# Kernel optimization log

Hardware: AMD Instinct MI355X
Metric: run time of the kernel (lower is better)

## Reference

```python
import jax, jax.numpy as jnp
import numpy as np

CTX = 768   # ctx_len in the original module
C = 768     # n_embd
B = 16
T = 768
K_EPS = 1e-8


def setup_inputs() -> dict:
    key = jax.random.key(0)
    ks = jax.random.split(key, 10)
    scale = 1.0 / np.sqrt(C)
    x = jax.random.normal(ks[0], (B, T, C), jnp.float32)
    time_decay = jax.random.normal(ks[1], (C, 1), jnp.float32) * 0.1
    time_first = jnp.full((C, 1), np.log(0.3), jnp.float32)
    time_mix_k = jax.random.uniform(ks[2], (1, 1, C), jnp.float32)
    time_mix_v = jax.random.uniform(ks[3], (1, 1, C), jnp.float32)
    time_mix_r = jax.random.uniform(ks[4], (1, 1, C), jnp.float32)
    Wk = jax.random.normal(ks[5], (C, C), jnp.float32) * scale
    Wv = jax.random.normal(ks[6], (C, C), jnp.float32) * scale
    Wr = jax.random.normal(ks[7], (C, C), jnp.float32) * scale
    Wo = jax.random.normal(ks[8], (C, C), jnp.float32) * scale
    return {"x": x, "time_decay": time_decay, "time_first": time_first,
            "time_mix_k": time_mix_k, "time_mix_v": time_mix_v, "time_mix_r": time_mix_r,
            "Wk": Wk, "Wv": Wv, "Wr": Wr, "Wo": Wo}


def reference(x, time_decay, time_first, time_mix_k, time_mix_v, time_mix_r, Wk, Wv, Wr, Wo):
    Bb, Tt, Cc = x.shape
    # time_shift: xx[t] = x[t-1], xx[0] = 0
    xx = jnp.pad(x, ((0, 0), (1, 0), (0, 0)))[:, :Tt]
    xk = x * time_mix_k + xx * (1.0 - time_mix_k)
    xv = x * time_mix_v + xx * (1.0 - time_mix_v)
    xr = x * time_mix_r + xx * (1.0 - time_mix_r)
    # projections (nn.Linear, no bias: y = x @ W.T); k, v laid out [B, C, T]
    k = jnp.einsum('btc,oc->bot', xk, Wk)
    v = jnp.einsum('btc,oc->bot', xv, Wv)
    r = jnp.einsum('btc,oc->bto', xr, Wr)
    k = jnp.exp(jnp.minimum(k, 60.0))
    kv = k * v
    # decay kernel: time_w = cat([exp(time_decay)*time_curve, time_first]); w = exp(time_w)[:, -T:]
    curve = (jnp.arange(CTX - 1) - (CTX - 2)).astype(x.dtype)  # [-(CTX-2) .. 0]
    tw = jnp.concatenate([jnp.exp(time_decay) * curve[None, :], time_first], axis=-1)  # [C, CTX]
    w = jnp.exp(tw)[:, -Tt:]            # [C, T]
    kern = w[:, None, :]                # [C, 1, T] depthwise kernel

    def causal_conv(z):  # z: [B, C, T] -> [B, C, T], left-padded cross-correlation
        return jax.lax.conv_general_dilated(
            z, kern, window_strides=(1,), padding=[(Tt - 1, 0)],
            feature_group_count=Cc, dimension_numbers=('NCH', 'OIH', 'NCH'))

    wkv = causal_conv(kv)
    wk = causal_conv(k) + K_EPS
    rwkv = jax.nn.sigmoid(r) * jnp.transpose(wkv / wk, (0, 2, 1))  # [B, T, C]
    return jnp.einsum('btc,oc->bto', rwkv, Wo)
```

## Files before the change

### kernel.cpp

```cpp
#include <hip/hip_runtime.h>
#include <math.h>

#define Mq 12288
#define Nq 768
#define Kq 768
#define Tq 768
#define Bq 16
#define Cq 768
#define BK 64

typedef __bf16 bf16x8 __attribute__((ext_vector_type(8)));
typedef __bf16 bf16x4 __attribute__((ext_vector_type(4)));
typedef float  floatx4 __attribute__((ext_vector_type(4)));

#define GLD_LDS16(g, l) __builtin_amdgcn_global_load_lds(                      \
    (const __attribute__((address_space(1))) unsigned int*)(g),                \
    (__attribute__((address_space(3))) unsigned int*)(l), 16, 0, 0)

__global__ __launch_bounds__(256)
void prep_w(const float* __restrict__ Wk, const float* __restrict__ Wv,
            const float* __restrict__ Wr, const float* __restrict__ Wo,
            __bf16* __restrict__ o)
{
    const int i   = blockIdx.x * 256 + threadIdx.x;
    const int a   = i / 147456;
    const int off = (i - a * 147456) * 4;
    const float* s = (a == 0) ? Wk : (a == 1) ? Wv : (a == 2) ? Wr : Wo;
    const float4 v = *(const float4*)(s + off);
    bf16x4 r = { (__bf16)v.x, (__bf16)v.y, (__bf16)v.z, (__bf16)v.w };
    *(bf16x4*)(o + (size_t)a * 589824 + off) = r;
}

__global__ __launch_bounds__(256)
void prep_mix(const float* __restrict__ x,
              const float* __restrict__ mk, const float* __restrict__ mv,
              const float* __restrict__ mr,
              __bf16* __restrict__ xk, __bf16* __restrict__ xv,
              __bf16* __restrict__ xr)
{
    const int i  = blockIdx.x * 256 + threadIdx.x;
    const int c4 = i % (Cq / 4);
    const int m  = i / (Cq / 4);
    const int t  = m % Tq;
    const int c0 = c4 * 4;

    const float4 xc = *(const float4*)(x + (size_t)m * Cq + c0);
    float4 xp = make_float4(0.f, 0.f, 0.f, 0.f);
    if (t > 0) xp = *(const float4*)(x + (size_t)(m - 1) * Cq + c0);

    const float4 k4 = *(const float4*)(mk + c0);
    const float4 v4 = *(const float4*)(mv + c0);
    const float4 r4 = *(const float4*)(mr + c0);

    bf16x4 ok = { (__bf16)fmaf(k4.x, xc.x - xp.x, xp.x),
                  (__bf16)fmaf(k4.y, xc.y - xp.y, xp.y),
                  (__bf16)fmaf(k4.z, xc.z - xp.z, xp.z),
                  (__bf16)fmaf(k4.w, xc.w - xp.w, xp.w) };
    bf16x4 ov = { (__bf16)fmaf(v4.x, xc.x - xp.x, xp.x),
                  (__bf16)fmaf(v4.y, xc.y - xp.y, xp.y),
                  (__bf16)fmaf(v4.z, xc.z - xp.z, xp.z),
                  (__bf16)fmaf(v4.w, xc.w - xp.w, xp.w) };
    bf16x4 orr = { (__bf16)fmaf(r4.x, xc.x - xp.x, xp.x),
                   (__bf16)fmaf(r4.y, xc.y - xp.y, xp.y),
                   (__bf16)fmaf(r4.z, xc.z - xp.z, xp.z),
                   (__bf16)fmaf(r4.w, xc.w - xp.w, xp.w) };
    const size_t o = (size_t)m * Cq + c0;
    *(bf16x4*)(xk + o) = ok;
    *(bf16x4*)(xv + o) = ov;
    *(bf16x4*)(xr + o) = orr;
}

template<bool KVR>
__global__ __launch_bounds__(256)
void mfma_gemm(const __bf16* __restrict__ A0, const __bf16* __restrict__ A1,
               const __bf16* __restrict__ A2,
               const __bf16* __restrict__ W,
               __bf16* __restrict__ OUTb,
               float*  __restrict__ OUTf)
{
    __shared__ __bf16 As[128 * BK];
    __shared__ __bf16 Bs[128 * BK];

    const int tid   = threadIdx.x;
    const int wave  = tid >> 6;
    const int lane  = tid & 63;
    const int m0    = blockIdx.y * 128;
    const int nb    = blockIdx.x;
    const int matid = KVR ? nb / 6 : 0;
    const int n0    = KVR ? (nb % 6) * 128 : nb * 128;
    const int wn0   = nb * 128;

    const __bf16* A = KVR ? (matid == 0 ? A0 : matid == 1 ? A1 : A2) : A0;

    const int r8 = lane >> 3;
    const int cc = lane & 7;
    const int sc = cc ^ r8;
    const __bf16* gA[4];
    const __bf16* gB[4];
    __bf16* lA[4];
    __bf16* lB[4];
#pragma unroll
    for (int i = 0; i < 4; ++i) {
        const int row = (wave * 4 + i) * 8 + r8;
        gA[i] = A + (size_t)(m0  + row) * Kq + sc * 8;
        gB[i] = W + (size_t)(wn0 + row) * Kq + sc * 8;
        lA[i] = As + (wave * 4 + i) * 512;
        lB[i] = Bs + (wave * 4 + i) * 512;
    }

    const int qr = wave >> 1, qc = wave & 1;
    const int rowA = qr * 64 + (lane & 15);
    const int rowB = qc * 64 + (lane & 15);
    const int lk   = lane >> 4;

    floatx4 acc[4][4];
#pragma unroll
    for (int i = 0; i < 4; ++i)
#pragma unroll
        for (int j = 0; j < 4; ++j) acc[i][j] = (floatx4){0.f, 0.f, 0.f, 0.f};

    for (int kt = 0; kt < Kq / BK; ++kt) {
#pragma unroll
        for (int i = 0; i < 4; ++i) {
            GLD_LDS16(gA[i], lA[i]);
            GLD_LDS16(gB[i], lB[i]);
            gA[i] += BK; gB[i] += BK;
        }
        __syncthreads();

#pragma unroll
        for (int kk = 0; kk < 2; ++kk) {
            bf16x8 aF[4], bF[4];
#pragma unroll
            for (int i = 0; i < 4; ++i) {
                const int ra = rowA + i * 16;
                aF[i] = *(const bf16x8*)(As + ra * BK +
                                         (((kk << 2) | lk) ^ (ra & 7)) * 8);
            }
#pragma unroll
            for (int j = 0; j < 4; ++j) {
                const int rb = rowB + j * 16;
                bF[j] = *(const bf16x8*)(Bs + rb * BK +
                                         (((kk << 2) | lk) ^ (rb & 7)) * 8);
            }
#pragma unroll
            for (int i = 0; i < 4; ++i)
#pragma unroll
                for (int j = 0; j < 4; ++j)
                    acc[i][j] = __builtin_amdgcn_mfma_f32_16x16x32_bf16(
                        aF[i], bF[j], acc[i][j], 0, 0, 0);
        }
        __syncthreads();
    }

    const int er = qr * 64 + (lane >> 4) * 4;
    const int ec = qc * 64 + (lane & 15);
#pragma unroll
    for (int i = 0; i < 4; ++i) {
#pragma unroll
        for (int j = 0; j < 4; ++j) {
            const int n = n0 + ec + j * 16;
#pragma unroll
            for (int reg = 0; reg < 4; ++reg) {
                const int m = m0 + er + i * 16 + reg;
                float v = acc[i][j][reg];
                if (KVR) {
                    if (matid == 0)      v = expf(fminf(v, 60.f));
                    else if (matid == 2) v = 1.f / (1.f + expf(-v));
                    OUTb[(size_t)matid * Mq * Nq + (size_t)m * Nq + n] = (__bf16)v;
                } else {
                    OUTf[(size_t)m * Nq + n] = v;
                }
            }
        }
    }
}

#define SEG 8
#define SLEN (Tq / SEG)

__global__ __launch_bounds__(512)
void scan_kernel(const __bf16* __restrict__ kb, const __bf16* __restrict__ vb,
                 __bf16* rb,
                 const float* __restrict__ td, const float* __restrict__ tf)
{
    __shared__ float aS[SEG][64];
    __shared__ float bS[SEG][64];

    const int cx  = threadIdx.x;
    const int seg = threadIdx.y;
    const int c   = blockIdx.x * 64 + cx;
    const int b   = blockIdx.y;

    const float d  = expf(td[c]);
    const float wd = expf(-d);
    const float u  = expf(tf[c]);

    const size_t base = ((size_t)b * Tq + seg * SLEN) * Cq + c;

    float a = 0.f, bs = 0.f;
    for (int t = 0; t < SLEN; ++t) {
        const size_t idx = base + (size_t)t * Cq;
        const float kt = (float)kb[idx];
        const float vt = (float)vb[idx];
        a  = fmaf(wd, a, kt * vt);
        bs = fmaf(wd, bs, kt);
    }
    aS[seg][cx] = a;
    bS[seg][cx] = bs;
    __syncthreads();

    if (seg == 0) {
        const float w96 = expf(-d * (float)SLEN);
        float ina = 0.f, inb = 0.f;
#pragma unroll
        for (int s = 0; s < SEG; ++s) {
            const float ta = aS[s][cx];
            const float tb = bS[s][cx];
            aS[s][cx] = ina;
            bS[s][cx] = inb;
            ina = fmaf(w96, ina, ta);
            inb = fmaf(w96, inb, tb);
        }
    }
    __syncthreads();

    a  = aS[seg][cx];
    bs = bS[seg][cx];
    for (int t = 0; t < SLEN; ++t) {
        const size_t idx = base + (size_t)t * Cq;
        const float kt = (float)kb[idx];
        const float vt = (float)vb[idx];
        const float sr = (float)rb[idx];
        const float kv = kt * vt;
        const float num = fmaf(u, kv, a);
        const float den = fmaf(u, kt, bs) + 1e-8f;
        rb[idx] = (__bf16)(sr * num / den);
        a  = fmaf(wd, a, kv);
        bs = fmaf(wd, bs, kt);
    }
}

extern "C" void kernel_launch(void* const* d_in, const int* in_sizes, int n_in,
                              void* d_out, int out_size, void* d_ws, size_t ws_size,
                              hipStream_t stream)
{
    const float* x  = (const float*)d_in[0];
    const float* td = (const float*)d_in[1];
    const float* tf = (const float*)d_in[2];
    const float* mk = (const float*)d_in[3];
    const float* mv = (const float*)d_in[4];
    const float* mr = (const float*)d_in[5];
    const float* Wk = (const float*)d_in[6];
    const float* Wv = (const float*)d_in[7];
    const float* Wr = (const float*)d_in[8];
    const float* Wo = (const float*)d_in[9];

    const size_t MC = (size_t)Mq * Cq;

    __bf16* xk = (__bf16*)d_out;
    __bf16* xv = xk + MC;

    __bf16* xr   = (__bf16*)d_ws;
    __bf16* kbuf = xr + MC;
    __bf16* vbuf = kbuf + MC;
    __bf16* rbuf = vbuf + MC;
    __bf16* Wp   = rbuf + MC;
    __bf16* Wob  = Wp + 3 * 589824;

    prep_w<<<2304, 256, 0, stream>>>(Wk, Wv, Wr, Wo, Wp);
    prep_mix<<<(Mq * (Cq / 4)) / 256, 256, 0, stream>>>(x, mk, mv, mr, xk, xv, xr);

    mfma_gemm<true><<<dim3(18, 96), 256, 0, stream>>>(
        xk, xv, xr, Wp, kbuf, nullptr);

    scan_kernel<<<dim3(Cq / 64, Bq), dim3(64, SEG), 0, stream>>>(
        kbuf, vbuf, rbuf, td, tf);

    mfma_gemm<false><<<dim3(6, 96), 256, 0, stream>>>(
        rbuf, nullptr, nullptr, Wob, nullptr, (float*)d_out);
}
```

Baseline: 255.1 us.

## Merge prep kernels, shrink GEMM M-tile, vectorize epilogue and scan

The two preprocessing kernels are merged into one launch. The GEMM M-tile shrinks from 128 to 64 with a launch-bounds occupancy hint of 6, and the operands are swapped so each lane stores a vector of four contiguous channels instead of scalars. The scan processes two channels per thread with bf16x2 loads and uses 16 segments instead of 8. The aim is more parallelism and occupancy and wider memory accesses, at the cost of lower per-block data reuse in the GEMM.

```diff
diff --git a/kernel.cpp b/kernel.cpp
--- a/kernel.cpp
+++ b/kernel.cpp
@@ -8,9 +8,11 @@
 #define Bq 16
 #define Cq 768
 #define BK 64
+#define BM 64
 
 typedef __bf16 bf16x8 __attribute__((ext_vector_type(8)));
 typedef __bf16 bf16x4 __attribute__((ext_vector_type(4)));
+typedef __bf16 bf16x2 __attribute__((ext_vector_type(2)));
 typedef float  floatx4 __attribute__((ext_vector_type(4)));
 
 #define GLD_LDS16(g, l) __builtin_amdgcn_global_load_lds(                      \
@@ -18,73 +20,71 @@
     (__attribute__((address_space(3))) unsigned int*)(l), 16, 0, 0)
 
 __global__ __launch_bounds__(256)
-void prep_w(const float* __restrict__ Wk, const float* __restrict__ Wv,
-            const float* __restrict__ Wr, const float* __restrict__ Wo,
-            __bf16* __restrict__ o)
-{
-    const int i   = blockIdx.x * 256 + threadIdx.x;
-    const int a   = i / 147456;
-    const int off = (i - a * 147456) * 4;
-    const float* s = (a == 0) ? Wk : (a == 1) ? Wv : (a == 2) ? Wr : Wo;
-    const float4 v = *(const float4*)(s + off);
-    bf16x4 r = { (__bf16)v.x, (__bf16)v.y, (__bf16)v.z, (__bf16)v.w };
-    *(bf16x4*)(o + (size_t)a * 589824 + off) = r;
-}
-
-__global__ __launch_bounds__(256)
-void prep_mix(const float* __restrict__ x,
-              const float* __restrict__ mk, const float* __restrict__ mv,
-              const float* __restrict__ mr,
-              __bf16* __restrict__ xk, __bf16* __restrict__ xv,
-              __bf16* __restrict__ xr)
-{
-    const int i  = blockIdx.x * 256 + threadIdx.x;
-    const int c4 = i % (Cq / 4);
-    const int m  = i / (Cq / 4);
-    const int t  = m % Tq;
-    const int c0 = c4 * 4;
-
-    const float4 xc = *(const float4*)(x + (size_t)m * Cq + c0);
-    float4 xp = make_float4(0.f, 0.f, 0.f, 0.f);
-    if (t > 0) xp = *(const float4*)(x + (size_t)(m - 1) * Cq + c0);
-
-    const float4 k4 = *(const float4*)(mk + c0);
-    const float4 v4 = *(const float4*)(mv + c0);
-    const float4 r4 = *(const float4*)(mr + c0);
-
-    bf16x4 ok = { (__bf16)fmaf(k4.x, xc.x - xp.x, xp.x),
-                  (__bf16)fmaf(k4.y, xc.y - xp.y, xp.y),
-                  (__bf16)fmaf(k4.z, xc.z - xp.z, xp.z),
-                  (__bf16)fmaf(k4.w, xc.w - xp.w, xp.w) };
-    bf16x4 ov = { (__bf16)fmaf(v4.x, xc.x - xp.x, xp.x),
-                  (__bf16)fmaf(v4.y, xc.y - xp.y, xp.y),
-                  (__bf16)fmaf(v4.z, xc.z - xp.z, xp.z),
-                  (__bf16)fmaf(v4.w, xc.w - xp.w, xp.w) };
-    bf16x4 orr = { (__bf16)fmaf(r4.x, xc.x - xp.x, xp.x),
-                   (__bf16)fmaf(r4.y, xc.y - xp.y, xp.y),
-                   (__bf16)fmaf(r4.z, xc.z - xp.z, xp.z),
-                   (__bf16)fmaf(r4.w, xc.w - xp.w, xp.w) };
-    const size_t o = (size_t)m * Cq + c0;
-    *(bf16x4*)(xk + o) = ok;
-    *(bf16x4*)(xv + o) = ov;
-    *(bf16x4*)(xr + o) = orr;
+void prep_kernel(const float* __restrict__ x,
+                 const float* __restrict__ mk, const float* __restrict__ mv,
+                 const float* __restrict__ mr,
+                 const float* __restrict__ Wk, const float* __restrict__ Wv,
+                 const float* __restrict__ Wr, const float* __restrict__ Wo,
+                 __bf16* __restrict__ xk, __bf16* __restrict__ xv,
+                 __bf16* __restrict__ xr, __bf16* __restrict__ wp)
+{
+    const int bid = blockIdx.x;
+    if (bid < 9216) {
+        const int i  = bid * 256 + threadIdx.x;
+        const int c4 = i % (Cq / 4);
+        const int m  = i / (Cq / 4);
+        const int t  = m % Tq;
+        const int c0 = c4 * 4;
+
+        const float4 xc = *(const float4*)(x + (size_t)m * Cq + c0);
+        float4 xp = make_float4(0.f, 0.f, 0.f, 0.f);
+        if (t > 0) xp = *(const float4*)(x + (size_t)(m - 1) * Cq + c0);
+
+        const float4 k4 = *(const float4*)(mk + c0);
+        const float4 v4 = *(const float4*)(mv + c0);
+        const float4 r4 = *(const float4*)(mr + c0);
+
+        bf16x4 ok = { (__bf16)fmaf(k4.x, xc.x - xp.x, xp.x),
+                      (__bf16)fmaf(k4.y, xc.y - xp.y, xp.y),
+                      (__bf16)fmaf(k4.z, xc.z - xp.z, xp.z),
+                      (__bf16)fmaf(k4.w, xc.w - xp.w, xp.w) };
+        bf16x4 ov = { (__bf16)fmaf(v4.x, xc.x - xp.x, xp.x),
+                      (__bf16)fmaf(v4.y, xc.y - xp.y, xp.y),
+                      (__bf16)fmaf(v4.z, xc.z - xp.z, xp.z),
+                      (__bf16)fmaf(v4.w, xc.w - xp.w, xp.w) };
+        bf16x4 orr = { (__bf16)fmaf(r4.x, xc.x - xp.x, xp.x),
+                       (__bf16)fmaf(r4.y, xc.y - xp.y, xp.y),
+                       (__bf16)fmaf(r4.z, xc.z - xp.z, xp.z),
+                       (__bf16)fmaf(r4.w, xc.w - xp.w, xp.w) };
+        const size_t o = (size_t)m * Cq + c0;
+        *(bf16x4*)(xk + o) = ok;
+        *(bf16x4*)(xv + o) = ov;
+        *(bf16x4*)(xr + o) = orr;
+    } else {
+        const int i   = (bid - 9216) * 256 + threadIdx.x;
+        const int a   = i / 147456;
+        const int off = (i - a * 147456) * 4;
+        const float* s = (a == 0) ? Wk : (a == 1) ? Wv : (a == 2) ? Wr : Wo;
+        const float4 v = *(const float4*)(s + off);
+        bf16x4 r = { (__bf16)v.x, (__bf16)v.y, (__bf16)v.z, (__bf16)v.w };
+        *(bf16x4*)(wp + (size_t)a * 589824 + off) = r;
+    }
 }
 
 template<bool KVR>
-__global__ __launch_bounds__(256)
+__global__ __launch_bounds__(256, 6)
 void mfma_gemm(const __bf16* __restrict__ A0, const __bf16* __restrict__ A1,
                const __bf16* __restrict__ A2,
                const __bf16* __restrict__ W,
-               __bf16* __restrict__ OUTb,
-               float*  __restrict__ OUTf)
-{
-    __shared__ __bf16 As[128 * BK];
+               __bf16* __restrict__ OUTb, float* __restrict__ OUTf)
+{
+    __shared__ __bf16 As[BM * BK];
     __shared__ __bf16 Bs[128 * BK];
 
     const int tid   = threadIdx.x;
     const int wave  = tid >> 6;
     const int lane  = tid & 63;
-    const int m0    = blockIdx.y * 128;
+    const int m0    = blockIdx.y * BM;
     const int nb    = blockIdx.x;
     const int matid = KVR ? nb / 6 : 0;
     const int n0    = KVR ? (nb % 6) * 128 : nb * 128;
@@ -93,151 +93,166 @@
     const __bf16* A = KVR ? (matid == 0 ? A0 : matid == 1 ? A1 : A2) : A0;
 
     const int r8 = lane >> 3;
-    const int cc = lane & 7;
-    const int sc = cc ^ r8;
-    const __bf16* gA[4];
-    const __bf16* gB[4];
-    __bf16* lA[4];
-    __bf16* lB[4];
+    const int sc = (lane & 7) ^ r8;
+    const __bf16* gA[2];  __bf16* lA[2];
+    const __bf16* gB[4];  __bf16* lB[4];
+#pragma unroll
+    for (int i = 0; i < 2; ++i) {
+        const int row = (wave * 2 + i) * 8 + r8;
+        gA[i] = A + (size_t)(m0 + row) * Kq + sc * 8;
+        lA[i] = As + (wave * 2 + i) * 512;
+    }
 #pragma unroll
     for (int i = 0; i < 4; ++i) {
         const int row = (wave * 4 + i) * 8 + r8;
-        gA[i] = A + (size_t)(m0  + row) * Kq + sc * 8;
         gB[i] = W + (size_t)(wn0 + row) * Kq + sc * 8;
-        lA[i] = As + (wave * 4 + i) * 512;
         lB[i] = Bs + (wave * 4 + i) * 512;
     }
 
-    const int qr = wave >> 1, qc = wave & 1;
-    const int rowA = qr * 64 + (lane & 15);
-    const int rowB = qc * 64 + (lane & 15);
+    const int qm = wave & 1;
+    const int qn = wave >> 1;
+    const int xRow = qm * 32 + (lane & 15);
+    const int wRow = qn * 64 + (lane & 15);
     const int lk   = lane >> 4;
 
-    floatx4 acc[4][4];
+    floatx4 acc[4][2];
 #pragma unroll
     for (int i = 0; i < 4; ++i)
 #pragma unroll
-        for (int j = 0; j < 4; ++j) acc[i][j] = (floatx4){0.f, 0.f, 0.f, 0.f};
+        for (int j = 0; j < 2; ++j) acc[i][j] = (floatx4){0.f, 0.f, 0.f, 0.f};
 
     for (int kt = 0; kt < Kq / BK; ++kt) {
 #pragma unroll
-        for (int i = 0; i < 4; ++i) {
-            GLD_LDS16(gA[i], lA[i]);
-            GLD_LDS16(gB[i], lB[i]);
-            gA[i] += BK; gB[i] += BK;
+        for (int i = 0; i < 2; ++i) { GLD_LDS16(gA[i], lA[i]); gA[i] += BK; }
+#pragma unroll
+        for (int i = 0; i < 4; ++i) { GLD_LDS16(gB[i], lB[i]); gB[i] += BK; }
+        __syncthreads();
+
+#pragma unroll
+        for (int kk = 0; kk < 2; ++kk) {
+            bf16x8 wF[4], xF[2];
+#pragma unroll
+            for (int i = 0; i < 4; ++i) {
+                const int r = wRow + i * 16;
+                wF[i] = *(const bf16x8*)(Bs + r * BK +
+                                         (((kk << 2) | lk) ^ (r & 7)) * 8);
+            }
+#pragma unroll
+            for (int j = 0; j < 2; ++j) {
+                const int r = xRow + j * 16;
+                xF[j] = *(const bf16x8*)(As + r * BK +
+                                         (((kk << 2) | lk) ^ (r & 7)) * 8);
+            }
+#pragma unroll
+            for (int i = 0; i < 4; ++i)
+#pragma unroll
+                for (int j = 0; j < 2; ++j)
+                    acc[i][j] = __builtin_amdgcn_mfma_f32_16x16x32_bf16(
+                        wF[i], xF[j], acc[i][j], 0, 0, 0);
         }
         __syncthreads();
-
-#pragma unroll
-        for (int kk = 0; kk < 2; ++kk) {
-            bf16x8 aF[4], bF[4];
-#pragma unroll
-            for (int i = 0; i < 4; ++i) {
-                const int ra = rowA + i * 16;
-                aF[i] = *(const bf16x8*)(As + ra * BK +
-                                         (((kk << 2) | lk) ^ (ra & 7)) * 8);
-            }
-#pragma unroll
-            for (int j = 0; j < 4; ++j) {
-                const int rb = rowB + j * 16;
-                bF[j] = *(const bf16x8*)(Bs + rb * BK +
-                                         (((kk << 2) | lk) ^ (rb & 7)) * 8);
-            }
-#pragma unroll
-            for (int i = 0; i < 4; ++i)
-#pragma unroll
-                for (int j = 0; j < 4; ++j)
-                    acc[i][j] = __builtin_amdgcn_mfma_f32_16x16x32_bf16(
-                        aF[i], bF[j], acc[i][j], 0, 0, 0);
-        }
-        __syncthreads();
-    }
-
-    const int er = qr * 64 + (lane >> 4) * 4;
-    const int ec = qc * 64 + (lane & 15);
-#pragma unroll
-    for (int i = 0; i < 4; ++i) {
-#pragma unroll
-        for (int j = 0; j < 4; ++j) {
-            const int n = n0 + ec + j * 16;
-#pragma unroll
-            for (int reg = 0; reg < 4; ++reg) {
-                const int m = m0 + er + i * 16 + reg;
-                float v = acc[i][j][reg];
-                if (KVR) {
-                    if (matid == 0)      v = expf(fminf(v, 60.f));
-                    else if (matid == 2) v = 1.f / (1.f + expf(-v));
-                    OUTb[(size_t)matid * Mq * Nq + (size_t)m * Nq + n] = (__bf16)v;
-                } else {
-                    OUTf[(size_t)m * Nq + n] = v;
+    }
+
+#pragma unroll
+    for (int j = 0; j < 2; ++j) {
+        const int tok = m0 + qm * 32 + j * 16 + (lane & 15);
+#pragma unroll
+        for (int i = 0; i < 4; ++i) {
+            const int ch = n0 + qn * 64 + i * 16 + (lane >> 4) * 4;
+            if (KVR) {
+                float v0 = acc[i][j][0], v1 = acc[i][j][1];
+                float v2 = acc[i][j][2], v3 = acc[i][j][3];
+                if (matid == 0) {
+                    v0 = expf(fminf(v0, 60.f)); v1 = expf(fminf(v1, 60.f));
+                    v2 = expf(fminf(v2, 60.f)); v3 = expf(fminf(v3, 60.f));
+                } else if (matid == 2) {
+                    v0 = 1.f / (1.f + expf(-v0)); v1 = 1.f / (1.f + expf(-v1));
+                    v2 = 1.f / (1.f + expf(-v2)); v3 = 1.f / (1.f + expf(-v3));
                 }
+                bf16x4 o = { (__bf16)v0, (__bf16)v1, (__bf16)v2, (__bf16)v3 };
+                *(bf16x4*)(OUTb + (size_t)matid * Mq * Nq +
+                           (size_t)tok * Nq + ch) = o;
+            } else {
+                floatx4 o = acc[i][j];
+                *(floatx4*)(OUTf + (size_t)tok * Nq + ch) = o;
             }
         }
     }
 }
 
-#define SEG 8
+#define SEG 16
 #define SLEN (Tq / SEG)
 
-__global__ __launch_bounds__(512)
+__global__ __launch_bounds__(1024)
 void scan_kernel(const __bf16* __restrict__ kb, const __bf16* __restrict__ vb,
                  __bf16* rb,
                  const float* __restrict__ td, const float* __restrict__ tf)
 {
-    __shared__ float aS[SEG][64];
-    __shared__ float bS[SEG][64];
+    __shared__ float2 aS[SEG][64];
+    __shared__ float2 bS[SEG][64];
 
     const int cx  = threadIdx.x;
     const int seg = threadIdx.y;
-    const int c   = blockIdx.x * 64 + cx;
+    const int c0  = blockIdx.x * 128 + cx * 2;
     const int b   = blockIdx.y;
 
-    const float d  = expf(td[c]);
-    const float wd = expf(-d);
-    const float u  = expf(tf[c]);
-
-    const size_t base = ((size_t)b * Tq + seg * SLEN) * Cq + c;
-
-    float a = 0.f, bs = 0.f;
+    const float d0 = expf(td[c0]),     d1 = expf(td[c0 + 1]);
+    const float w0 = expf(-d0),        w1 = expf(-d1);
+    const float u0 = expf(tf[c0]),     u1 = expf(tf[c0 + 1]);
+
+    const size_t base = ((size_t)b * Tq + seg * SLEN) * Cq + c0;
+
+    float a0 = 0.f, a1 = 0.f, s0 = 0.f, s1 = 0.f;
+#pragma unroll 4
     for (int t = 0; t < SLEN; ++t) {
         const size_t idx = base + (size_t)t * Cq;
-        const float kt = (float)kb[idx];
-        const float vt = (float)vb[idx];
-        a  = fmaf(wd, a, kt * vt);
-        bs = fmaf(wd, bs, kt);
-    }
-    aS[seg][cx] = a;
-    bS[seg][cx] = bs;
+        const bf16x2 k2 = *(const bf16x2*)(kb + idx);
+        const bf16x2 v2 = *(const bf16x2*)(vb + idx);
+        const float k0 = (float)k2[0], k1 = (float)k2[1];
+        a0 = fmaf(w0, a0, k0 * (float)v2[0]);
+        a1 = fmaf(w1, a1, k1 * (float)v2[1]);
+        s0 = fmaf(w0, s0, k0);
+        s1 = fmaf(w1, s1, k1);
+    }
+    aS[seg][cx] = make_float2(a0, a1);
+    bS[seg][cx] = make_float2(s0, s1);
     __syncthreads();
 
     if (seg == 0) {
-        const float w96 = expf(-d * (float)SLEN);
-        float ina = 0.f, inb = 0.f;
+        const float W0 = expf(-d0 * (float)SLEN);
+        const float W1 = expf(-d1 * (float)SLEN);
+        float ia0 = 0.f, ia1 = 0.f, ib0 = 0.f, ib1 = 0.f;
 #pragma unroll
         for (int s = 0; s < SEG; ++s) {
-            const float ta = aS[s][cx];
-            const float tb = bS[s][cx];
-            aS[s][cx] = ina;
-            bS[s][cx] = inb;
-            ina = fmaf(w96, ina, ta);
-            inb = fmaf(w96, inb, tb);
+            const float2 ta = aS[s][cx];
+            const float2 tb = bS[s][cx];
+            aS[s][cx] = make_float2(ia0, ia1);
+            bS[s][cx] = make_float2(ib0, ib1);
+            ia0 = fmaf(W0, ia0, ta.x);  ia1 = fmaf(W1, ia1, ta.y);
+            ib0 = fmaf(W0, ib0, tb.x);  ib1 = fmaf(W1, ib1, tb.y);
         }
     }
     __syncthreads();
 
-    a  = aS[seg][cx];
-    bs = bS[seg][cx];
+    const float2 ain = aS[seg][cx];
+    const float2 bin = bS[seg][cx];
+    a0 = ain.x; a1 = ain.y; s0 = bin.x; s1 = bin.y;
+#pragma unroll 2
     for (int t = 0; t < SLEN; ++t) {
         const size_t idx = base + (size_t)t * Cq;
-        const float kt = (float)kb[idx];
-        const float vt = (float)vb[idx];
-        const float sr = (float)rb[idx];
-        const float kv = kt * vt;
-        const float num = fmaf(u, kv, a);
-        const float den = fmaf(u, kt, bs) + 1e-8f;
-        rb[idx] = (__bf16)(sr * num / den);
-        a  = fmaf(wd, a, kv);
-        bs = fmaf(wd, bs, kt);
+        const bf16x2 k2 = *(const bf16x2*)(kb + idx);
+        const bf16x2 v2 = *(const bf16x2*)(vb + idx);
+        const bf16x2 r2 = *(const bf16x2*)(rb + idx);
+        const float k0 = (float)k2[0], k1 = (float)k2[1];
+        const float kv0 = k0 * (float)v2[0], kv1 = k1 * (float)v2[1];
+        const float n0 = fmaf(u0, kv0, a0), n1 = fmaf(u1, kv1, a1);
+        const float e0 = fmaf(u0, k0, s0) + 1e-8f;
+        const float e1 = fmaf(u1, k1, s1) + 1e-8f;
+        bf16x2 o = { (__bf16)((float)r2[0] * n0 / e0),
+                     (__bf16)((float)r2[1] * n1 / e1) };
+        *(bf16x2*)(rb + idx) = o;
+        a0 = fmaf(w0, a0, kv0);  a1 = fmaf(w1, a1, kv1);
+        s0 = fmaf(w0, s0, k0);   s1 = fmaf(w1, s1, k1);
     }
 }
 
@@ -268,15 +283,15 @@
     __bf16* Wp   = rbuf + MC;
     __bf16* Wob  = Wp + 3 * 589824;
 
-    prep_w<<<2304, 256, 0, stream>>>(Wk, Wv, Wr, Wo, Wp);
-    prep_mix<<<(Mq * (Cq / 4)) / 256, 256, 0, stream>>>(x, mk, mv, mr, xk, xv, xr);
-
-    mfma_gemm<true><<<dim3(18, 96), 256, 0, stream>>>(
+    prep_kernel<<<11520, 256, 0, stream>>>(x, mk, mv, mr, Wk, Wv, Wr, Wo,
+                                           xk, xv, xr, Wp);
+
+    mfma_gemm<true><<<dim3(18, Mq / BM), 256, 0, stream>>>(
         xk, xv, xr, Wp, kbuf, nullptr);
 
-    scan_kernel<<<dim3(Cq / 64, Bq), dim3(64, SEG), 0, stream>>>(
+    scan_kernel<<<dim3(Cq / 128, Bq), dim3(64, SEG), 0, stream>>>(
         kbuf, vbuf, rbuf, td, tf);
 
-    mfma_gemm<false><<<dim3(6, 96), 256, 0, stream>>>(
+    mfma_gemm<false><<<dim3(6, Mq / BM), 256, 0, stream>>>(
         rbuf, nullptr, nullptr, Wob, nullptr, (float*)d_out);
 }
```

After: 243.6 us. 1.05x faster.
